# Kernel optimization log

Hardware: AMD Instinct MI355X
Metric: run time of the kernel (lower is better)

## Reference

```python
import jax, jax.numpy as jnp
import numpy as np

# SamplesLoss('sinkhorn', p=2, blur=0.05, scaling=0.5, diameter=2.0, debias=True, backend='tensorized')
P = 2
BLUR = 0.05
SCALING = 0.5
DIAMETER = 2.0


def epsilon_schedule(p, diameter, blur, scaling):
    # geomloss epsilon annealing: diameter^p -> blur^p, geometric in eps
    eps_list = (
        [diameter ** p]
        + [np.exp(e) for e in np.arange(p * np.log(diameter), p * np.log(blur), p * np.log(scaling))]
        + [blur ** p]
    )
    return [float(e) for e in eps_list]


def softmin(eps, C, h):
    # soft C-transform: f_i = -eps * log sum_j exp(h_j - C_ij/eps)
    # C: (B,N,M), h: (B,M) -> (B,N)
    return -eps * jax.scipy.special.logsumexp(h[:, None, :] - C / eps, axis=2)


def sq_cost(x, y):
    # SqDist(x,y)/2 : (B,N,D),(B,M,D) -> (B,N,M)
    x2 = jnp.sum(x * x, axis=-1)[:, :, None]
    y2 = jnp.sum(y * y, axis=-1)[:, None, :]
    return (x2 + y2 - 2.0 * jnp.einsum('bnd,bmd->bnm', x, y)) * 0.5


def setup_inputs() -> dict:
    key = jax.random.key(0)
    k1, k2 = jax.random.split(key)
    x = jax.random.uniform(k1, (8, 2048, 3), dtype=jnp.float32)
    y = jax.random.uniform(k2, (8, 2048, 3), dtype=jnp.float32)
    return {"x": x, "y": y}


def reference(x, y):
    B, N, _ = x.shape
    M = y.shape[1]
    # uniform weights (SamplesLoss default when only point clouds are given)
    a_log = jnp.full((B, N), -float(np.log(N)), dtype=x.dtype)
    b_log = jnp.full((B, M), -float(np.log(M)), dtype=y.dtype)

    C_xy = sq_cost(x, y)                 # (B,N,M)
    C_yx = jnp.swapaxes(C_xy, 1, 2)      # (B,M,N)
    C_xx = sq_cost(x, x)                 # (B,N,N) debias term
    C_yy = sq_cost(y, y)                 # (B,M,M) debias term

    eps_list = epsilon_schedule(P, DIAMETER, BLUR, SCALING)

    # initialization at the coarsest temperature (balanced OT: damping = 1)
    eps0 = eps_list[0]
    f_aa = softmin(eps0, C_xx, a_log)
    g_bb = softmin(eps0, C_yy, b_log)
    g_ab = softmin(eps0, C_yx, a_log)
    f_ba = softmin(eps0, C_xy, b_log)

    # symmetric Sinkhorn loop with epsilon scaling (no grad tracked in torch here)
    for eps in eps_list:
        ft_ba = softmin(eps, C_xy, b_log + g_ab / eps)
        gt_ab = softmin(eps, C_yx, a_log + f_ba / eps)
        f_ba = 0.5 * (f_ba + ft_ba)
        g_ab = 0.5 * (g_ab + gt_ab)
        ft_aa = softmin(eps, C_xx, a_log + f_aa / eps)
        gt_bb = softmin(eps, C_yy, b_log + g_bb / eps)
        f_aa = 0.5 * (f_aa + ft_aa)
        g_bb = 0.5 * (g_bb + gt_bb)

    # last extrapolation step, with detached dual potentials (torch .detach())
    eps = eps_list[-1]
    sg = jax.lax.stop_gradient
    f_ba, g_ab = (
        softmin(eps, C_xy, b_log + sg(g_ab) / eps),
        softmin(eps, C_yx, a_log + sg(f_ba) / eps),
    )
    f_aa = softmin(eps, C_xx, a_log + sg(f_aa) / eps)
    g_bb = softmin(eps, C_yy, b_log + sg(g_bb) / eps)

    # debiased Sinkhorn divergence, batch mode -> (B,)
    a = jnp.exp(a_log)
    b = jnp.exp(b_log)
    return jnp.sum(a * (f_ba - f_aa), axis=-1) + jnp.sum(b * (g_ab - g_bb), axis=-1)
```

## Files before the change

kernel.cpp:

```cpp
#include <hip/hip_runtime.h>
#include <math.h>

#define BATCH 8
#define NPTS 2048
#define THREADS 256
#define HALF_COLS 1024
#define TILES_H 32
#define ROWS_PER_BLOCK 64
#define LOG_M 7.62559580411076

typedef __attribute__((ext_vector_type(8)))  __bf16 bf16x8;
typedef __attribute__((ext_vector_type(16))) float  f32x16;

union FragU { unsigned short u[8]; uint4 v; };

__device__ __forceinline__ unsigned short f2bf(float f) {
    union { float f; unsigned u; } x; x.f = f;
    unsigned r = x.u + 0x7FFFu + ((x.u >> 16) & 1u);
    return (unsigned short)(r >> 16);
}
__device__ __forceinline__ float bf2f(unsigned short b) {
    union { unsigned u; float f; } x; x.u = ((unsigned)b) << 16;
    return x.f;
}

__global__ __launch_bounds__(THREADS) void softmin_pass(
    const float* __restrict__ x, const float* __restrict__ y,
    const float* __restrict__ potSrc, float* __restrict__ potDst,
    float sigma, float k2, float inv_k2, float rowc0, int avg)
{
    __shared__ uint4 BF[TILES_H][64];
    __shared__ uint4 AF[2][64];
    __shared__ float NM[ROWS_PER_BLOCK];
    __shared__ float SRED[2][2][32];

    const int type  = blockIdx.z;
    const int batch = blockIdx.y;

    const float* rowP;
    const float* colP;
    int hslot, oslot;
    if (type == 0)      { rowP = x; colP = y; hslot = 1; oslot = 0; }
    else if (type == 1) { rowP = y; colP = x; hslot = 0; oslot = 1; }
    else if (type == 2) { rowP = x; colP = x; hslot = 2; oslot = 2; }
    else                { rowP = y; colP = y; hslot = 3; oslot = 3; }

    rowP += batch * NPTS * 3;
    colP += batch * NPTS * 3;
    const float* hP   = potSrc + (hslot * BATCH + batch) * NPTS;
    const float* oldP = potSrc + (oslot * BATCH + batch) * NPTS;
    float*       outP = potDst + (oslot * BATCH + batch) * NPTS;

    if (threadIdx.x < 128) {
        const int g = threadIdx.x >> 6, idx = threadIdx.x & 63;
        const int row = blockIdx.x * ROWS_PER_BLOCK + g * 32 + (idx & 31);
        float x0 = rowP[3 * row + 0], x1 = rowP[3 * row + 1], x2 = rowP[3 * row + 2];
        float p0 = sigma * (x0 - 0.5f), p1 = sigma * (x1 - 0.5f), p2 = sigma * (x2 - 0.5f);
        unsigned short h0 = f2bf(p0); unsigned short l0 = f2bf(p0 - bf2f(h0));
        unsigned short h1 = f2bf(p1); unsigned short l1 = f2bf(p1 - bf2f(h1));
        unsigned short h2 = f2bf(p2); unsigned short l2 = f2bf(p2 - bf2f(h2));
        FragU f;
        if (idx < 32) {
            f.u[0] = h0; f.u[1] = h0; f.u[2] = l0; f.u[3] = l0;
            f.u[4] = h1; f.u[5] = h1; f.u[6] = l1; f.u[7] = l1;
        } else {
            f.u[0] = h2; f.u[1] = h2; f.u[2] = l2; f.u[3] = l2;
            f.u[4] = 0x3F80; f.u[5] = 0x3F80; f.u[6] = 0x3F80; f.u[7] = 0;
        }
        AF[g][idx] = f.v;
    } else if (threadIdx.x < 128 + ROWS_PER_BLOCK) {
        const int r = threadIdx.x - 128;
        const int i = blockIdx.x * ROWS_PER_BLOCK + r;
        float x0 = rowP[3 * i + 0], x1 = rowP[3 * i + 1], x2 = rowP[3 * i + 2];
        float p0 = x0 - 0.5f, p1 = x1 - 0.5f, p2 = x2 - 0.5f;
        float rowconst = 0.5f * (p0 * p0 + p1 * p1 + p2 * p2) + rowc0;
        NM[r] = (oldP[i] - rowconst) * inv_k2;
    }

    const int lane = threadIdx.x & 63;
    const int wave = threadIdx.x >> 6;
    const int g    = wave >> 1;
    const int c    = wave & 1;
    const int khalf = lane >> 5;

    float s[16];
    #pragma unroll
    for (int r = 0; r < 16; ++r) s[r] = 0.0f;
    bf16x8 af;
    f32x16 nmv;

    for (int h = 0; h < 2; ++h) {
        if (h) __syncthreads();

        for (int jj = threadIdx.x; jj < HALF_COLS; jj += THREADS) {
            const int j = h * HALF_COLS + jj;
            float y0 = colP[3 * j + 0], y1 = colP[3 * j + 1], y2 = colP[3 * j + 2];
            float p0 = y0 - 0.5f, p1 = y1 - 0.5f, p2 = y2 - 0.5f;
            unsigned short h0 = f2bf(p0); unsigned short l0 = f2bf(p0 - bf2f(h0));
            unsigned short h1 = f2bf(p1); unsigned short l1 = f2bf(p1 - bf2f(h1));
            unsigned short h2 = f2bf(p2); unsigned short l2 = f2bf(p2 - bf2f(h2));
            float hhe = sigma * (hP[j] - 0.5f * (p0 * p0 + p1 * p1 + p2 * p2));
            unsigned short hA = f2bf(hhe); float r1 = hhe - bf2f(hA);
            unsigned short hB = f2bf(r1);  float r2 = r1 - bf2f(hB);
            unsigned short hC = f2bf(r2);
            FragU f0, f1;
            f0.u[0] = h0; f0.u[1] = l0; f0.u[2] = h0; f0.u[3] = l0;
            f0.u[4] = h1; f0.u[5] = l1; f0.u[6] = h1; f0.u[7] = l1;
            f1.u[0] = h2; f1.u[1] = l2; f1.u[2] = h2; f1.u[3] = l2;
            f1.u[4] = hA; f1.u[5] = hB; f1.u[6] = hC; f1.u[7] = 0;
            BF[jj >> 5][jj & 31]        = f0.v;
            BF[jj >> 5][32 + (jj & 31)] = f1.v;
        }
        __syncthreads();

        if (h == 0) {
            af = *(const bf16x8*)&AF[g][lane];
            #pragma unroll
            for (int r = 0; r < 16; ++r) {
                const int row = (r & 3) + 8 * (r >> 2) + 4 * khalf;
                nmv[r] = NM[g * 32 + row];
            }
        }

        const int tbase = c * (TILES_H / 2);
        #pragma unroll 2
        for (int t = 0; t < TILES_H / 2; ++t) {
            bf16x8 bf = *(const bf16x8*)&BF[tbase + t][lane];
            f32x16 acc = __builtin_amdgcn_mfma_f32_32x32x16_bf16(af, bf, nmv, 0, 0, 0);
            #pragma unroll
            for (int r = 0; r < 16; ++r)
                s[r] += __builtin_amdgcn_exp2f(acc[r]);
        }
    }

    #pragma unroll
    for (int off = 1; off <= 16; off <<= 1)
        #pragma unroll
        for (int r = 0; r < 16; ++r)
            s[r] += __shfl_xor(s[r], off, 64);

    if ((lane & 31) == 0) {
        #pragma unroll
        for (int r = 0; r < 16; ++r) {
            const int row = (r & 3) + 8 * (r >> 2) + 4 * khalf;
            SRED[g][c][row] = s[r];
        }
    }
    __syncthreads();

    if (threadIdx.x < ROWS_PER_BLOCK) {
        const int p = threadIdx.x >> 5, r = threadIdx.x & 31;
        const int i = blockIdx.x * ROWS_PER_BLOCK + p * 32 + r;
        float sum = SRED[p][0][r] + SRED[p][1][r];
        float oldv = oldP[i];
        float res = oldv - k2 * __log2f(sum);
        outP[i] = avg ? 0.5f * (oldv + res) : res;
    }
}

__global__ void reduce_out(const float* __restrict__ pot, float* __restrict__ out)
{
    const int batch = blockIdx.x;
    const float* fba = pot + (0 * BATCH + batch) * NPTS;
    const float* gab = pot + (1 * BATCH + batch) * NPTS;
    const float* faa = pot + (2 * BATCH + batch) * NPTS;
    const float* gbb = pot + (3 * BATCH + batch) * NPTS;

    float s = 0.0f;
    for (int i = threadIdx.x; i < NPTS; i += blockDim.x)
        s += (fba[i] - faa[i]) + (gab[i] - gbb[i]);

    #pragma unroll
    for (int off = 32; off >= 1; off >>= 1)
        s += __shfl_xor(s, off, 64);

    __shared__ float red[THREADS / 64];
    const int lane = threadIdx.x & 63;
    const int wave = threadIdx.x >> 6;
    if (lane == 0) red[wave] = s;
    __syncthreads();
    if (threadIdx.x == 0) {
        float t = 0.0f;
        for (int w = 0; w < THREADS / 64; ++w) t += red[w];
        out[batch] = t * (1.0f / NPTS);
    }
}

extern "C" void kernel_launch(void* const* d_in, const int* in_sizes, int n_in,
                              void* d_out, int out_size, void* d_ws, size_t ws_size,
                              hipStream_t stream)
{
    const float* x = (const float*)d_in[0];
    const float* y = (const float*)d_in[1];
    float* out = (float*)d_out;

    const size_t potElems = (size_t)4 * BATCH * NPTS;
    float* P0 = (float*)d_ws;
    float* P1 = P0 + potElems;

    hipMemsetAsync(P0, 0, potElems * sizeof(float), stream);

    double epsl[16];
    int ne = 0;
    epsl[ne++] = 4.0;
    const double stop = 2.0 * log(0.05);
    const double step = 2.0 * log(0.5);
    for (double e = 2.0 * log(2.0); e > stop; e += step)
        epsl[ne++] = exp(e);
    epsl[ne++] = 0.05 * 0.05;

    float* src = P0;
    float* dst = P1;
    dim3 grid(NPTS / ROWS_PER_BLOCK, BATCH, 4);

    auto launch = [&](double eps, int avg) {
        float sigma  = (float)(M_LOG2E / eps);
        float k2     = (float)(eps * M_LN2);
        float inv_k2 = (float)(1.0 / (eps * M_LN2));
        float rowc0  = (float)(eps * LOG_M);
        softmin_pass<<<grid, THREADS, 0, stream>>>(
            x, y, src, dst, sigma, k2, inv_k2, rowc0, avg);
        float* t = src; src = dst; dst = t;
    };

    launch(epsl[0], 0);
    for (int k = 0; k < ne; ++k)
        launch(epsl[k], 1);
    launch(epsl[ne - 1], 0);

    reduce_out<<<dim3(BATCH), THREADS, 0, stream>>>(src, out);
}
```

Baseline: 268.1 us.

## Fuse all Sinkhorn passes into one persistent cooperative kernel with grid sync

Replaces the ten separate softmin kernel launches, the memset and the final reduction with a single cooperative kernel. Each block loops over logical tiles and the passes are separated by grid-wide syncs. The epsilon schedule is hardcoded and the zero initial potentials are substituted inline. This removes per-launch overhead and the memset, but adds grid barrier cost, and block count is capped by occupancy, assuming 256 CUs.

```diff
diff --git a/kernel.cpp b/kernel.cpp
--- a/kernel.cpp
+++ b/kernel.cpp
@@ -1,5 +1,8 @@
 #include <hip/hip_runtime.h>
+#include <hip/hip_cooperative_groups.h>
 #include <math.h>
+
+namespace cg = cooperative_groups;
 
 #define BATCH 8
 #define NPTS 2048
@@ -7,6 +10,7 @@
 #define HALF_COLS 1024
 #define TILES_H 32
 #define ROWS_PER_BLOCK 64
+#define NLOGICAL 1024
 #define LOG_M 7.62559580411076
 
 typedef __attribute__((ext_vector_type(8)))  __bf16 bf16x8;
@@ -24,165 +28,183 @@
     return x.f;
 }
 
-__global__ __launch_bounds__(THREADS) void softmin_pass(
+__global__ __launch_bounds__(THREADS) void sinkhorn_fused(
     const float* __restrict__ x, const float* __restrict__ y,
-    const float* __restrict__ potSrc, float* __restrict__ potDst,
-    float sigma, float k2, float inv_k2, float rowc0, int avg)
+    float* __restrict__ P0, float* __restrict__ P1, float* __restrict__ out)
 {
+    cg::grid_group gg = cg::this_grid();
+
     __shared__ uint4 BF[TILES_H][64];
     __shared__ uint4 AF[2][64];
     __shared__ float NM[ROWS_PER_BLOCK];
     __shared__ float SRED[2][2][32];
 
-    const int type  = blockIdx.z;
-    const int batch = blockIdx.y;
-
-    const float* rowP;
-    const float* colP;
-    int hslot, oslot;
-    if (type == 0)      { rowP = x; colP = y; hslot = 1; oslot = 0; }
-    else if (type == 1) { rowP = y; colP = x; hslot = 0; oslot = 1; }
-    else if (type == 2) { rowP = x; colP = x; hslot = 2; oslot = 2; }
-    else                { rowP = y; colP = y; hslot = 3; oslot = 3; }
-
-    rowP += batch * NPTS * 3;
-    colP += batch * NPTS * 3;
-    const float* hP   = potSrc + (hslot * BATCH + batch) * NPTS;
-    const float* oldP = potSrc + (oslot * BATCH + batch) * NPTS;
-    float*       outP = potDst + (oslot * BATCH + batch) * NPTS;
-
-    if (threadIdx.x < 128) {
-        const int g = threadIdx.x >> 6, idx = threadIdx.x & 63;
-        const int row = blockIdx.x * ROWS_PER_BLOCK + g * 32 + (idx & 31);
-        float x0 = rowP[3 * row + 0], x1 = rowP[3 * row + 1], x2 = rowP[3 * row + 2];
-        float p0 = sigma * (x0 - 0.5f), p1 = sigma * (x1 - 0.5f), p2 = sigma * (x2 - 0.5f);
-        unsigned short h0 = f2bf(p0); unsigned short l0 = f2bf(p0 - bf2f(h0));
-        unsigned short h1 = f2bf(p1); unsigned short l1 = f2bf(p1 - bf2f(h1));
-        unsigned short h2 = f2bf(p2); unsigned short l2 = f2bf(p2 - bf2f(h2));
-        FragU f;
-        if (idx < 32) {
-            f.u[0] = h0; f.u[1] = h0; f.u[2] = l0; f.u[3] = l0;
-            f.u[4] = h1; f.u[5] = h1; f.u[6] = l1; f.u[7] = l1;
-        } else {
-            f.u[0] = h2; f.u[1] = h2; f.u[2] = l2; f.u[3] = l2;
-            f.u[4] = 0x3F80; f.u[5] = 0x3F80; f.u[6] = 0x3F80; f.u[7] = 0;
+    const int lane  = threadIdx.x & 63;
+    const int wave  = threadIdx.x >> 6;
+    const int g     = wave >> 1;
+    const int c     = wave & 1;
+    const int khalf = lane >> 5;
+
+    const float epsR[10] = {4.0f, 4.0f, 4.0f, 1.0f, 0.25f, 0.0625f,
+                            0.015625f, 0.00390625f, 0.0025f, 0.0025f};
+
+    for (int r = 0; r < 10; ++r) {
+        const float eps    = epsR[r];
+        const float sigma  = (float)M_LOG2E / eps;
+        const float k2     = eps * (float)M_LN2;
+        const float inv_k2 = 1.0f / k2;
+        const float rowc0  = eps * (float)LOG_M;
+        const int   avg    = (r >= 1 && r <= 8);
+        float*       dst = (r & 1) ? P1 : P0;
+        const float* src = (r & 1) ? P0 : P1;
+
+        for (int lb = blockIdx.x; lb < NLOGICAL; lb += gridDim.x) {
+            const int xblk  = lb & 31;
+            const int batch = (lb >> 5) & 7;
+            const int type  = lb >> 8;
+
+            const float* rowP;
+            const float* colP;
+            int hslot, oslot;
+            if (type == 0)      { rowP = x; colP = y; hslot = 1; oslot = 0; }
+            else if (type == 1) { rowP = y; colP = x; hslot = 0; oslot = 1; }
+            else if (type == 2) { rowP = x; colP = x; hslot = 2; oslot = 2; }
+            else                { rowP = y; colP = y; hslot = 3; oslot = 3; }
+
+            rowP += batch * NPTS * 3;
+            colP += batch * NPTS * 3;
+            const float* hP   = src + (hslot * BATCH + batch) * NPTS;
+            const float* oldP = src + (oslot * BATCH + batch) * NPTS;
+            float*       outP = dst + (oslot * BATCH + batch) * NPTS;
+
+            __syncthreads();
+
+            if (threadIdx.x < 128) {
+                const int ag = threadIdx.x >> 6, idx = threadIdx.x & 63;
+                const int row = xblk * ROWS_PER_BLOCK + ag * 32 + (idx & 31);
+                float x0 = rowP[3 * row + 0], x1 = rowP[3 * row + 1], x2 = rowP[3 * row + 2];
+                float p0 = sigma * (x0 - 0.5f), p1 = sigma * (x1 - 0.5f), p2 = sigma * (x2 - 0.5f);
+                unsigned short h0 = f2bf(p0); unsigned short l0 = f2bf(p0 - bf2f(h0));
+                unsigned short h1 = f2bf(p1); unsigned short l1 = f2bf(p1 - bf2f(h1));
+                unsigned short h2 = f2bf(p2); unsigned short l2 = f2bf(p2 - bf2f(h2));
+                FragU f;
+                if (idx < 32) {
+                    f.u[0] = h0; f.u[1] = h0; f.u[2] = l0; f.u[3] = l0;
+                    f.u[4] = h1; f.u[5] = h1; f.u[6] = l1; f.u[7] = l1;
+                } else {
+                    f.u[0] = h2; f.u[1] = h2; f.u[2] = l2; f.u[3] = l2;
+                    f.u[4] = 0x3F80; f.u[5] = 0x3F80; f.u[6] = 0x3F80; f.u[7] = 0;
+                }
+                AF[ag][idx] = f.v;
+            } else if (threadIdx.x < 128 + ROWS_PER_BLOCK) {
+                const int rr = threadIdx.x - 128;
+                const int i = xblk * ROWS_PER_BLOCK + rr;
+                float x0 = rowP[3 * i + 0], x1 = rowP[3 * i + 1], x2 = rowP[3 * i + 2];
+                float p0 = x0 - 0.5f, p1 = x1 - 0.5f, p2 = x2 - 0.5f;
+                float rowconst = 0.5f * (p0 * p0 + p1 * p1 + p2 * p2) + rowc0;
+                float oldv = r ? oldP[i] : 0.0f;
+                NM[rr] = (oldv - rowconst) * inv_k2;
+            }
+
+            float s[16];
+            #pragma unroll
+            for (int q = 0; q < 16; ++q) s[q] = 0.0f;
+            bf16x8 af;
+            f32x16 nmv;
+
+            for (int h = 0; h < 2; ++h) {
+                if (h) __syncthreads();
+
+                for (int jj = threadIdx.x; jj < HALF_COLS; jj += THREADS) {
+                    const int j = h * HALF_COLS + jj;
+                    float y0 = colP[3 * j + 0], y1 = colP[3 * j + 1], y2 = colP[3 * j + 2];
+                    float p0 = y0 - 0.5f, p1 = y1 - 0.5f, p2 = y2 - 0.5f;
+                    unsigned short h0 = f2bf(p0); unsigned short l0 = f2bf(p0 - bf2f(h0));
+                    unsigned short h1 = f2bf(p1); unsigned short l1 = f2bf(p1 - bf2f(h1));
+                    unsigned short h2 = f2bf(p2); unsigned short l2 = f2bf(p2 - bf2f(h2));
+                    float pot = r ? hP[j] : 0.0f;
+                    float hhe = sigma * (pot - 0.5f * (p0 * p0 + p1 * p1 + p2 * p2));
+                    unsigned short hA = f2bf(hhe); float r1 = hhe - bf2f(hA);
+                    unsigned short hB = f2bf(r1);  float r2 = r1 - bf2f(hB);
+                    unsigned short hC = f2bf(r2);
+                    FragU f0, f1;
+                    f0.u[0] = h0; f0.u[1] = l0; f0.u[2] = h0; f0.u[3] = l0;
+                    f0.u[4] = h1; f0.u[5] = l1; f0.u[6] = h1; f0.u[7] = l1;
+                    f1.u[0] = h2; f1.u[1] = l2; f1.u[2] = h2; f1.u[3] = l2;
+                    f1.u[4] = hA; f1.u[5] = hB; f1.u[6] = hC; f1.u[7] = 0;
+                    BF[jj >> 5][jj & 31]        = f0.v;
+                    BF[jj >> 5][32 + (jj & 31)] = f1.v;
+                }
+                __syncthreads();
+
+                if (h == 0) {
+                    af = *(const bf16x8*)&AF[g][lane];
+                    #pragma unroll
+                    for (int q = 0; q < 16; ++q) {
+                        const int row = (q & 3) + 8 * (q >> 2) + 4 * khalf;
+                        nmv[q] = NM[g * 32 + row];
+                    }
+                }
+
+                const int tbase = c * (TILES_H / 2);
+                #pragma unroll 2
+                for (int t = 0; t < TILES_H / 2; ++t) {
+                    bf16x8 bf = *(const bf16x8*)&BF[tbase + t][lane];
+                    f32x16 acc = __builtin_amdgcn_mfma_f32_32x32x16_bf16(af, bf, nmv, 0, 0, 0);
+                    #pragma unroll
+                    for (int q = 0; q < 16; ++q)
+                        s[q] += __builtin_amdgcn_exp2f(acc[q]);
+                }
+            }
+
+            #pragma unroll
+            for (int off = 1; off <= 16; off <<= 1)
+                #pragma unroll
+                for (int q = 0; q < 16; ++q)
+                    s[q] += __shfl_xor(s[q], off, 64);
+
+            if ((lane & 31) == 0) {
+                #pragma unroll
+                for (int q = 0; q < 16; ++q) {
+                    const int row = (q & 3) + 8 * (q >> 2) + 4 * khalf;
+                    SRED[g][c][row] = s[q];
+                }
+            }
+            __syncthreads();
+
+            if (threadIdx.x < ROWS_PER_BLOCK) {
+                const int p = threadIdx.x >> 5, rr = threadIdx.x & 31;
+                const int i = xblk * ROWS_PER_BLOCK + p * 32 + rr;
+                float sum = SRED[p][0][rr] + SRED[p][1][rr];
+                float oldv = r ? oldP[i] : 0.0f;
+                float res = oldv - k2 * __log2f(sum);
+                outP[i] = avg ? 0.5f * (oldv + res) : res;
+            }
         }
-        AF[g][idx] = f.v;
-    } else if (threadIdx.x < 128 + ROWS_PER_BLOCK) {
-        const int r = threadIdx.x - 128;
-        const int i = blockIdx.x * ROWS_PER_BLOCK + r;
-        float x0 = rowP[3 * i + 0], x1 = rowP[3 * i + 1], x2 = rowP[3 * i + 2];
-        float p0 = x0 - 0.5f, p1 = x1 - 0.5f, p2 = x2 - 0.5f;
-        float rowconst = 0.5f * (p0 * p0 + p1 * p1 + p2 * p2) + rowc0;
-        NM[r] = (oldP[i] - rowconst) * inv_k2;
+        gg.sync();
     }
 
-    const int lane = threadIdx.x & 63;
-    const int wave = threadIdx.x >> 6;
-    const int g    = wave >> 1;
-    const int c    = wave & 1;
-    const int khalf = lane >> 5;
-
-    float s[16];
-    #pragma unroll
-    for (int r = 0; r < 16; ++r) s[r] = 0.0f;
-    bf16x8 af;
-    f32x16 nmv;
-
-    for (int h = 0; h < 2; ++h) {
-        if (h) __syncthreads();
-
-        for (int jj = threadIdx.x; jj < HALF_COLS; jj += THREADS) {
-            const int j = h * HALF_COLS + jj;
-            float y0 = colP[3 * j + 0], y1 = colP[3 * j + 1], y2 = colP[3 * j + 2];
-            float p0 = y0 - 0.5f, p1 = y1 - 0.5f, p2 = y2 - 0.5f;
-            unsigned short h0 = f2bf(p0); unsigned short l0 = f2bf(p0 - bf2f(h0));
-            unsigned short h1 = f2bf(p1); unsigned short l1 = f2bf(p1 - bf2f(h1));
-            unsigned short h2 = f2bf(p2); unsigned short l2 = f2bf(p2 - bf2f(h2));
-            float hhe = sigma * (hP[j] - 0.5f * (p0 * p0 + p1 * p1 + p2 * p2));
-            unsigned short hA = f2bf(hhe); float r1 = hhe - bf2f(hA);
-            unsigned short hB = f2bf(r1);  float r2 = r1 - bf2f(hB);
-            unsigned short hC = f2bf(r2);
-            FragU f0, f1;
-            f0.u[0] = h0; f0.u[1] = l0; f0.u[2] = h0; f0.u[3] = l0;
-            f0.u[4] = h1; f0.u[5] = l1; f0.u[6] = h1; f0.u[7] = l1;
-            f1.u[0] = h2; f1.u[1] = l2; f1.u[2] = h2; f1.u[3] = l2;
-            f1.u[4] = hA; f1.u[5] = hB; f1.u[6] = hC; f1.u[7] = 0;
-            BF[jj >> 5][jj & 31]        = f0.v;
-            BF[jj >> 5][32 + (jj & 31)] = f1.v;
+    for (int b = blockIdx.x; b < BATCH; b += gridDim.x) {
+        const float* fba = P1 + (0 * BATCH + b) * NPTS;
+        const float* gab = P1 + (1 * BATCH + b) * NPTS;
+        const float* faa = P1 + (2 * BATCH + b) * NPTS;
+        const float* gbb = P1 + (3 * BATCH + b) * NPTS;
+
+        float s = 0.0f;
+        for (int i = threadIdx.x; i < NPTS; i += THREADS)
+            s += (fba[i] - faa[i]) + (gab[i] - gbb[i]);
+
+        #pragma unroll
+        for (int off = 32; off >= 1; off >>= 1)
+            s += __shfl_xor(s, off, 64);
+
+        __syncthreads();
+        if (lane == 0) NM[wave] = s;
+        __syncthreads();
+        if (threadIdx.x == 0) {
+            float t = NM[0] + NM[1] + NM[2] + NM[3];
+            out[b] = t * (1.0f / NPTS);
         }
-        __syncthreads();
-
-        if (h == 0) {
-            af = *(const bf16x8*)&AF[g][lane];
-            #pragma unroll
-            for (int r = 0; r < 16; ++r) {
-                const int row = (r & 3) + 8 * (r >> 2) + 4 * khalf;
-                nmv[r] = NM[g * 32 + row];
-            }
-        }
-
-        const int tbase = c * (TILES_H / 2);
-        #pragma unroll 2
-        for (int t = 0; t < TILES_H / 2; ++t) {
-            bf16x8 bf = *(const bf16x8*)&BF[tbase + t][lane];
-            f32x16 acc = __builtin_amdgcn_mfma_f32_32x32x16_bf16(af, bf, nmv, 0, 0, 0);
-            #pragma unroll
-            for (int r = 0; r < 16; ++r)
-                s[r] += __builtin_amdgcn_exp2f(acc[r]);
-        }
-    }
-
-    #pragma unroll
-    for (int off = 1; off <= 16; off <<= 1)
-        #pragma unroll
-        for (int r = 0; r < 16; ++r)
-            s[r] += __shfl_xor(s[r], off, 64);
-
-    if ((lane & 31) == 0) {
-        #pragma unroll
-        for (int r = 0; r < 16; ++r) {
-            const int row = (r & 3) + 8 * (r >> 2) + 4 * khalf;
-            SRED[g][c][row] = s[r];
-        }
-    }
-    __syncthreads();
-
-    if (threadIdx.x < ROWS_PER_BLOCK) {
-        const int p = threadIdx.x >> 5, r = threadIdx.x & 31;
-        const int i = blockIdx.x * ROWS_PER_BLOCK + p * 32 + r;
-        float sum = SRED[p][0][r] + SRED[p][1][r];
-        float oldv = oldP[i];
-        float res = oldv - k2 * __log2f(sum);
-        outP[i] = avg ? 0.5f * (oldv + res) : res;
-    }
-}
-
-__global__ void reduce_out(const float* __restrict__ pot, float* __restrict__ out)
-{
-    const int batch = blockIdx.x;
-    const float* fba = pot + (0 * BATCH + batch) * NPTS;
-    const float* gab = pot + (1 * BATCH + batch) * NPTS;
-    const float* faa = pot + (2 * BATCH + batch) * NPTS;
-    const float* gbb = pot + (3 * BATCH + batch) * NPTS;
-
-    float s = 0.0f;
-    for (int i = threadIdx.x; i < NPTS; i += blockDim.x)
-        s += (fba[i] - faa[i]) + (gab[i] - gbb[i]);
-
-    #pragma unroll
-    for (int off = 32; off >= 1; off >>= 1)
-        s += __shfl_xor(s, off, 64);
-
-    __shared__ float red[THREADS / 64];
-    const int lane = threadIdx.x & 63;
-    const int wave = threadIdx.x >> 6;
-    if (lane == 0) red[wave] = s;
-    __syncthreads();
-    if (threadIdx.x == 0) {
-        float t = 0.0f;
-        for (int w = 0; w < THREADS / 64; ++w) t += red[w];
-        out[batch] = t * (1.0f / NPTS);
     }
 }
 
@@ -198,35 +220,14 @@
     float* P0 = (float*)d_ws;
     float* P1 = P0 + potElems;
 
-    hipMemsetAsync(P0, 0, potElems * sizeof(float), stream);
-
-    double epsl[16];
-    int ne = 0;
-    epsl[ne++] = 4.0;
-    const double stop = 2.0 * log(0.05);
-    const double step = 2.0 * log(0.5);
-    for (double e = 2.0 * log(2.0); e > stop; e += step)
-        epsl[ne++] = exp(e);
-    epsl[ne++] = 0.05 * 0.05;
-
-    float* src = P0;
-    float* dst = P1;
-    dim3 grid(NPTS / ROWS_PER_BLOCK, BATCH, 4);
-
-    auto launch = [&](double eps, int avg) {
-        float sigma  = (float)(M_LOG2E / eps);
-        float k2     = (float)(eps * M_LN2);
-        float inv_k2 = (float)(1.0 / (eps * M_LN2));
-        float rowc0  = (float)(eps * LOG_M);
-        softmin_pass<<<grid, THREADS, 0, stream>>>(
-            x, y, src, dst, sigma, k2, inv_k2, rowc0, avg);
-        float* t = src; src = dst; dst = t;
-    };
-
-    launch(epsl[0], 0);
-    for (int k = 0; k < ne; ++k)
-        launch(epsl[k], 1);
-    launch(epsl[ne - 1], 0);
-
-    reduce_out<<<dim3(BATCH), THREADS, 0, stream>>>(src, out);
-}
+    int maxB = 0;
+    if (hipOccupancyMaxActiveBlocksPerMultiprocessor(
+            &maxB, (const void*)sinkhorn_fused, THREADS, 0) != hipSuccess || maxB < 1)
+        maxB = 1;
+    int nblocks = maxB * 256;
+    if (nblocks > NLOGICAL) nblocks = NLOGICAL;
+
+    void* args[] = {(void*)&x, (void*)&y, (void*)&P0, (void*)&P1, (void*)&out};
+    hipLaunchCooperativeKernel((const void*)sinkhorn_fused,
+                               dim3(nblocks), dim3(THREADS), args, 0, stream);
+}
```

Result: slower. 765.8 us (+185.6%).
